# Optimization experiments

Hardware: AMD Instinct MI355X
Metric: run time of the kernel (lower is better)

The kernel has to match this reference:

```python
import jax, jax.numpy as jnp
import numpy as np


def _grid_sample_bilinear_zeros(img, grid):
    """PyTorch grid_sample(mode='bilinear', padding_mode='zeros', align_corners=True).
    img: (N, C, H, W); grid: (N, Ho, Wo, 2) with last dim = (x_norm, y_norm) in [-1, 1].
    """
    N, C, H, W = img.shape
    gx = (grid[..., 0] + 1.0) * 0.5 * (W - 1)  # (N, Ho, Wo) pixel coords
    gy = (grid[..., 1] + 1.0) * 0.5 * (H - 1)
    x0 = jnp.floor(gx)
    y0 = jnp.floor(gy)
    x1 = x0 + 1.0
    y1 = y0 + 1.0
    wx1 = gx - x0
    wx0 = 1.0 - wx1
    wy1 = gy - y0
    wy0 = 1.0 - wy1

    def corner(xi, yi, wgt):
        valid = ((xi >= 0) & (xi <= W - 1) & (yi >= 0) & (yi <= H - 1)).astype(img.dtype)
        xc = jnp.clip(xi, 0, W - 1).astype(jnp.int32)
        yc = jnp.clip(yi, 0, H - 1).astype(jnp.int32)
        # per-sample fancy gather: (C,H,W)[ :, (Ho,Wo), (Ho,Wo)] -> (C,Ho,Wo)
        v = jax.vmap(lambda im, yy, xx: im[:, yy, xx])(img, yc, xc)  # (N,C,Ho,Wo)
        return v * (valid * wgt)[:, None]

    return (corner(x0, y0, wx0 * wy0) + corner(x1, y0, wx1 * wy0)
            + corner(x0, y1, wx0 * wy1) + corner(x1, y1, wx1 * wy1))


def _backwarp(x, flow):
    """x, flow: (N, C/2, H, W); flow in pixels (hor, ver). align_corners=True grid."""
    N, _, H, W = flow.shape
    hor = jnp.linspace(-1.0, 1.0, W, dtype=flow.dtype)
    ver = jnp.linspace(-1.0, 1.0, H, dtype=flow.dtype)
    base = jnp.stack([jnp.broadcast_to(hor[None, :], (H, W)),
                      jnp.broadcast_to(ver[:, None], (H, W))], axis=0)[None]  # (1,2,H,W)
    # pixel flow -> normalized flow (H != W branch of original)
    norm = jnp.array([2.0 / (W - 1.0), 2.0 / (H - 1.0)], dtype=flow.dtype).reshape(1, 2, 1, 1)
    g = (base + flow * norm).transpose(0, 2, 3, 1)  # (N,H,W,2)
    return _grid_sample_bilinear_zeros(x, g)


def setup_inputs() -> dict:
    key = jax.random.key(0)
    k1, k2 = jax.random.split(key)
    B, C, T, H, W = 2, 3, 5, 720, 1280
    x = jax.random.normal(k1, (B, C, T, H, W), dtype=jnp.float32)
    f = jax.random.normal(k2, (B, 3, T, H, W), dtype=jnp.float32)
    return {"x": x, "f": f}


def reference(x, f):
    # scale = 1, num_seq = T (interpolate branch skipped since scale == 1)
    B, C, T, H, W = x.shape
    xf = x.transpose(0, 2, 1, 3, 4).reshape(B * T, C, H, W)      # (b t) c h w
    ff = f.transpose(0, 2, 1, 3, 4).reshape(B * T, 3, H, W)
    weight = jax.nn.sigmoid(ff[:, 2:3])                           # (BT,1,H,W)
    flow = ff[:, :2]                                              # (BT,2,H,W)
    xw = _backwarp(xf, flow)                                      # warped image
    ow = _backwarp(jnp.ones_like(xf), flow) * weight              # warped ones mask
    xw = xw * weight
    def back(a):  # (b t) c h w -> b c t h w
        return a.reshape(B, T, a.shape[1], H, W).transpose(0, 2, 1, 3, 4)
    return (back(ow), back(xw))
```

## Files before the change

### kernel.cpp

```cpp
#include <hip/hip_runtime.h>

typedef unsigned int u32;

constexpr int B  = 2, C = 3, T = 5, H = 720, W = 1280;
constexpr int HW = H * W;
constexpr int W2 = W / 2;
constexpr int P2 = B * T * H * W2;
constexpr int CH_STRIDE = T * HW;
constexpr int OUT_HALF  = B * C * T * HW;

__global__ __launch_bounds__(256)
void bwarp_kernel(const float* __restrict__ x, const float* __restrict__ f,
                  float* __restrict__ out)
{
    int i = blockIdx.x * 256 + threadIdx.x;
    if (i >= P2) return;

    int w2 = i % W2;
    int r  = i / W2;
    int h  = r % H;
    int bt = r / H;
    int b  = bt / T;
    int t  = bt - b * T;

    int plane = (b * 3 * T + t) * HW;
    int base0 = plane + h * W + 2 * w2;

    float2 fx2 = *(const float2*)(f + base0);
    float2 fy2 = *(const float2*)(f + base0 + CH_STRIDE);
    float2 fw2 = *(const float2*)(f + base0 + 2 * CH_STRIDE);

    float2 o0;
    float2 o1[3];

    #pragma unroll
    for (int j = 0; j < 2; ++j) {
        float fx = j ? fx2.y : fx2.x;
        float fy = j ? fy2.y : fy2.x;
        float fw = j ? fw2.y : fw2.x;

        float gx = (float)(2 * w2 + j) + fx;
        float gy = (float)h + fy;

        float x0f = floorf(gx), y0f = floorf(gy);
        float wx1 = gx - x0f, wx0 = 1.0f - wx1;
        float wy1 = gy - y0f, wy0 = 1.0f - wy1;
        int x0 = (int)x0f, y0 = (int)y0f;
        int x1 = x0 + 1,   y1 = y0 + 1;

        float vx0 = (x0 >= 0 && x0 < W) ? 1.0f : 0.0f;
        float vx1 = (x1 >= 0 && x1 < W) ? 1.0f : 0.0f;
        float vy0 = (y0 >= 0 && y0 < H) ? 1.0f : 0.0f;
        float vy1 = (y1 >= 0 && y1 < H) ? 1.0f : 0.0f;

        int x0c = min(max(x0, 0), W - 1);
        int x1c = min(max(x1, 0), W - 1);
        int y0c = min(max(y0, 0), H - 1);
        int y1c = min(max(y1, 0), H - 1);

        float w00 = wx0 * wy0 * vx0 * vy0;
        float w10 = wx1 * wy0 * vx1 * vy0;
        float w01 = wx0 * wy1 * vx0 * vy1;
        float w11 = wx1 * wy1 * vx1 * vy1;

        float sigw = 1.0f / (1.0f + __expf(-fw));

        float s0 = (w00 + w10 + w01 + w11) * sigw;
        if (j) o0.y = s0; else o0.x = s0;

        int r0 = y0c * W, r1 = y1c * W;
        int a00 = r0 + x0c, a10 = r0 + x1c;
        int a01 = r1 + x0c, a11 = r1 + x1c;

        #pragma unroll
        for (int c = 0; c < 3; ++c) {
            const float* xp = x + plane + c * CH_STRIDE;
            float v = (w00 * xp[a00] + w10 * xp[a10]
                     + w01 * xp[a01] + w11 * xp[a11]) * sigw;
            if (j) o1[c].y = v; else o1[c].x = v;
        }
    }

    #pragma unroll
    for (int c = 0; c < 3; ++c) {
        *(float2*)(out + base0 + c * CH_STRIDE) = o0;
        *(float2*)(out + OUT_HALF + base0 + c * CH_STRIDE) = o1[c];
    }
}

extern "C" void kernel_launch(void* const* d_in, const int* in_sizes, int n_in,
                              void* d_out, int out_size, void* d_ws, size_t ws_size,
                              hipStream_t stream) {
    const float* x = (const float*)d_in[0];
    const float* f = (const float*)d_in[1];
    float* out = (float*)d_out;
    int blocks = (P2 + 255) / 256;
    bwarp_kernel<<<blocks, 256, 0, stream>>>(x, f, out);
}
```

Baseline: 428.1 us.

## Widen to 4 pixels per thread, pair corner loads, and swizzle blocks across XCDs

Each thread now handles 4 pixels, so flow loads and output stores become float4. The two horizontal corners of each bilinear row are fetched with one unaligned float2 load, with selects covering the left and right edge cases. Block IDs are remapped so consecutive blocks land contiguously per XCD, aiming to improve L2 locality for the gathers. The cost is more registers per thread, fewer threads overall, and possibly slower unaligned 8-byte loads.

After: 425.1 us. No clear change (-0.7%).

```diff
diff --git a/kernel.cpp b/kernel.cpp
--- a/kernel.cpp
+++ b/kernel.cpp
@@ -4,42 +4,51 @@
 
 constexpr int B  = 2, C = 3, T = 5, H = 720, W = 1280;
 constexpr int HW = H * W;
-constexpr int W2 = W / 2;
-constexpr int P2 = B * T * H * W2;
+constexpr int W4 = W / 4;
+constexpr int P4 = B * T * H * W4;
 constexpr int CH_STRIDE = T * HW;
 constexpr int OUT_HALF  = B * C * T * HW;
+constexpr int NBLK  = P4 / 256;
+constexpr int NXCD  = 8;
+constexpr int CHUNK = NBLK / NXCD;
+
+typedef float2 __attribute__((aligned(4))) f2u;
 
 __global__ __launch_bounds__(256)
 void bwarp_kernel(const float* __restrict__ x, const float* __restrict__ f,
                   float* __restrict__ out)
 {
-    int i = blockIdx.x * 256 + threadIdx.x;
-    if (i >= P2) return;
+    int bid = blockIdx.x;
+    int swz = (bid & (NXCD - 1)) * CHUNK + (bid >> 3);
+    int i   = swz * 256 + (int)threadIdx.x;
+    if (i >= P4) return;
 
-    int w2 = i % W2;
-    int r  = i / W2;
-    int h  = r % H;
-    int bt = r / H;
-    int b  = bt / T;
-    int t  = bt - b * T;
+    int w4i = i % W4;
+    int r   = i / W4;
+    int h   = r % H;
+    int bt  = r / H;
+    int b   = bt / T;
+    int t   = bt - b * T;
 
     int plane = (b * 3 * T + t) * HW;
-    int base0 = plane + h * W + 2 * w2;
+    int base0 = plane + h * W + 4 * w4i;
 
-    float2 fx2 = *(const float2*)(f + base0);
-    float2 fy2 = *(const float2*)(f + base0 + CH_STRIDE);
-    float2 fw2 = *(const float2*)(f + base0 + 2 * CH_STRIDE);
+    float4 fx4 = *(const float4*)(f + base0);
+    float4 fy4 = *(const float4*)(f + base0 + CH_STRIDE);
+    float4 fw4 = *(const float4*)(f + base0 + 2 * CH_STRIDE);
 
-    float2 o0;
-    float2 o1[3];
+    const float* fxp = (const float*)&fx4;
+    const float* fyp = (const float*)&fy4;
+    const float* fwp = (const float*)&fw4;
+
+    float o0[4];
+    float o1[3][4];
 
     #pragma unroll
-    for (int j = 0; j < 2; ++j) {
-        float fx = j ? fx2.y : fx2.x;
-        float fy = j ? fy2.y : fy2.x;
-        float fw = j ? fw2.y : fw2.x;
+    for (int j = 0; j < 4; ++j) {
+        float fx = fxp[j], fy = fyp[j], fw = fwp[j];
 
-        float gx = (float)(2 * w2 + j) + fx;
+        float gx = (float)(4 * w4i + j) + fx;
         float gy = (float)h + fy;
 
         float x0f = floorf(gx), y0f = floorf(gy);
@@ -53,11 +62,6 @@
         float vy0 = (y0 >= 0 && y0 < H) ? 1.0f : 0.0f;
         float vy1 = (y1 >= 0 && y1 < H) ? 1.0f : 0.0f;
 
-        int x0c = min(max(x0, 0), W - 1);
-        int x1c = min(max(x1, 0), W - 1);
-        int y0c = min(max(y0, 0), H - 1);
-        int y1c = min(max(y1, 0), H - 1);
-
         float w00 = wx0 * wy0 * vx0 * vy0;
         float w10 = wx1 * wy0 * vx1 * vy0;
         float w01 = wx0 * wy1 * vx0 * vy1;
@@ -65,26 +69,36 @@
 
         float sigw = 1.0f / (1.0f + __expf(-fw));
 
-        float s0 = (w00 + w10 + w01 + w11) * sigw;
-        if (j) o0.y = s0; else o0.x = s0;
+        o0[j] = (w00 + w10 + w01 + w11) * sigw;
 
-        int r0 = y0c * W, r1 = y1c * W;
-        int a00 = r0 + x0c, a10 = r0 + x1c;
-        int a01 = r1 + x0c, a11 = r1 + x1c;
+        int xl  = min(max(x0, 0), W - 2);
+        int y0c = min(max(y0, 0), H - 1);
+        int y1c = min(max(y1, 0), H - 1);
+        bool hi0 = (x0 >= W - 1);
+        bool lo1 = (x0 < 0);
+
+        int a0 = y0c * W + xl;
+        int a1 = y1c * W + xl;
 
         #pragma unroll
         for (int c = 0; c < 3; ++c) {
             const float* xp = x + plane + c * CH_STRIDE;
-            float v = (w00 * xp[a00] + w10 * xp[a10]
-                     + w01 * xp[a01] + w11 * xp[a11]) * sigw;
-            if (j) o1[c].y = v; else o1[c].x = v;
+            f2u p0 = *(const f2u*)(xp + a0);
+            f2u p1 = *(const f2u*)(xp + a1);
+            float v00 = hi0 ? p0.y : p0.x;
+            float v10 = lo1 ? p0.x : p0.y;
+            float v01 = hi0 ? p1.y : p1.x;
+            float v11 = lo1 ? p1.x : p1.y;
+            o1[c][j] = (w00 * v00 + w10 * v10 + w01 * v01 + w11 * v11) * sigw;
         }
     }
 
+    float4 ow4 = make_float4(o0[0], o0[1], o0[2], o0[3]);
     #pragma unroll
     for (int c = 0; c < 3; ++c) {
-        *(float2*)(out + base0 + c * CH_STRIDE) = o0;
-        *(float2*)(out + OUT_HALF + base0 + c * CH_STRIDE) = o1[c];
+        *(float4*)(out + base0 + c * CH_STRIDE) = ow4;
+        float4 xw4 = make_float4(o1[c][0], o1[c][1], o1[c][2], o1[c][3]);
+        *(float4*)(out + OUT_HALF + base0 + c * CH_STRIDE) = xw4;
     }
 }
 
@@ -94,6 +108,5 @@
     const float* x = (const float*)d_in[0];
     const float* f = (const float*)d_in[1];
     float* out = (float*)d_out;
-    int blocks = (P2 + 255) / 256;
-    bwarp_kernel<<<blocks, 256, 0, stream>>>(x, f, out);
+    bwarp_kernel<<<NBLK, 256, 0, stream>>>(x, f, out);
 }
```
